# Kernel tuning notes

Hardware: AMD Instinct MI355X
Metric: run time of the kernel (lower is better)

## Reference

```python
import jax, jax.numpy as jnp
import numpy as np

B, H, L, N, F = 32, 256, 2048, 64, 32  # batch, d_model, seq len, d_state//2 complex modes, num_features


def setup_inputs() -> dict:
    key = jax.random.key(0)
    ks = jax.random.split(key, 16)
    inp = {
        "x": jax.random.normal(ks[0], (B, H, L), jnp.float32),
        "t": jax.random.normal(ks[1], (B, H), jnp.float32),
        "features": jax.random.normal(ks[2], (B, F, L), jnp.float32),
        # time_linear
        "Wt": jax.random.normal(ks[3], (H, H), jnp.float32) / np.sqrt(H),
        "bt": jnp.zeros((H,), jnp.float32),
        # LayerNorm over d_model
        "ln_g": jnp.ones((H,), jnp.float32),
        "ln_b": jnp.zeros((H,), jnp.float32),
        # S4 (diagonal / S4D parameterization, d_state=128 -> N=64 complex, bidirectional)
        "log_dt": jnp.log(jnp.full((H,), 0.01, jnp.float32))
                  + jax.random.uniform(ks[4], (H,), jnp.float32, -1.0, 1.0),
        "logA_real": jnp.log(0.5 * jnp.ones((H, N), jnp.float32)),
        "A_imag": jnp.broadcast_to(np.pi * jnp.arange(N, dtype=jnp.float32), (H, N)).copy(),
        "C_re": jax.random.normal(ks[5], (2, H, N), jnp.float32) / np.sqrt(2 * N),
        "C_im": jax.random.normal(ks[6], (2, H, N), jnp.float32) / np.sqrt(2 * N),
        "D": jax.random.normal(ks[7], (H,), jnp.float32),
        # S4 output position-wise linear
        "Wout": jax.random.normal(ks[8], (H, H), jnp.float32) / np.sqrt(H),
        "bout": jnp.zeros((H,), jnp.float32),
        # out_linear1 / out_linear2 (1x1 convs)
        "W1": jax.random.normal(ks[9], (H, H), jnp.float32) / np.sqrt(H),
        "b1": jnp.zeros((H,), jnp.float32),
        "W2": jax.random.normal(ks[10], (H, H), jnp.float32) / np.sqrt(H),
        "b2": jnp.zeros((H,), jnp.float32),
        # feature_encoder 1x1 conv
        "Wf": jax.random.normal(ks[11], (H, F), jnp.float32) / np.sqrt(F),
        "bf": jnp.zeros((H,), jnp.float32),
    }
    return inp


def _s4_block(x, t, features, Wt, bt, ln_g, ln_b, log_dt, logA_real, A_imag,
              C_re, C_im, D, Wout, bout, W1, b1, W2, b2, Wf, bf):
    Bb, Hh, Ll = x.shape
    # time conditioning: Linear(t) broadcast over length  -> (B,H,L)
    tb = t @ Wt.T + bt
    xin = x + tb[:, :, None]
    # LayerNorm over channel (d_model) axis (norm applied on transposed tensor)
    mu = jnp.mean(xin, axis=1, keepdims=True)
    var = jnp.var(xin, axis=1, keepdims=True)
    z = (xin - mu) / jnp.sqrt(var + 1e-5) * ln_g[None, :, None] + ln_b[None, :, None]
    # --- bidirectional S4 (diagonal SSM) kernel ---
    dt = jnp.exp(log_dt)                       # (H,)
    A = -jnp.exp(logA_real) + 1j * A_imag      # (H,N)
    dtA = dt[:, None] * A                      # (H,N)
    Cd = (C_re + 1j * C_im) * (jnp.exp(dtA) - 1.0) / A      # (2,H,N) discretized C
    vand = jnp.exp(dtA[:, :, None] * jnp.arange(Ll))         # (H,N,L) Vandermonde
    K = 2.0 * jnp.real(jnp.einsum('chn,hnl->chl', Cd, vand))  # (2,H,L)
    zeros = jnp.zeros_like(K[0])
    k = jnp.concatenate([K[0], zeros], -1) + jnp.concatenate([zeros, K[1][:, ::-1]], -1)  # (H,2L)
    # FFT global convolution
    y = jnp.fft.irfft(jnp.fft.rfft(z, 2 * Ll) * jnp.fft.rfft(k, 2 * Ll)[None], 2 * Ll)[..., :Ll]
    y = y + z * D[None, :, None]
    y = jax.nn.gelu(y)
    y = jnp.einsum('bhl,gh->bgl', y, Wout) + bout[None, :, None]
    xr = y + xin                                # residual inside S4Layer
    # feature encoder + gated activation
    out = xr + jnp.einsum('bfl,hf->bhl', features, Wf) + bf[None, :, None]
    g = jnp.tanh(out) * jax.nn.sigmoid(out)
    o1 = jnp.einsum('bhl,gh->bgl', g, W1) + b1[None, :, None]
    o2 = jnp.einsum('bhl,gh->bgl', g, W2) + b2[None, :, None]
    return (o1 + x, o2)


def reference(x, t, features, Wt, bt, ln_g, ln_b, log_dt, logA_real, A_imag,
              C_re, C_im, D, Wout, bout, W1, b1, W2, b2, Wf, bf):
    return _s4_block(x, t, features, Wt, bt, ln_g, ln_b, log_dt, logA_real, A_imag,
                     C_re, C_im, D, Wout, bout, W1, b1, W2, b2, Wf, bf)
```

## Files before the change

### kernel.cpp

```cpp
#include <hip/hip_runtime.h>

typedef unsigned short ushort_t;

#define Bb 32
#define Hh 256
#define Ll 2048
#define Nn 64
#define BHL 16777216

typedef __bf16 bf16x8 __attribute__((ext_vector_type(8)));
typedef float f32x4 __attribute__((ext_vector_type(4)));
typedef unsigned int uint4v __attribute__((ext_vector_type(4)));

__device__ __forceinline__ ushort_t f2bf(float f) {
    unsigned int u = __float_as_uint(f);
    unsigned int r = ((u >> 16) & 1u) + 0x7fffu;
    return (ushort_t)((u + r) >> 16);
}
__device__ __forceinline__ float bf2f(ushort_t h) {
    return __uint_as_float(((unsigned int)h) << 16);
}
__device__ __forceinline__ float gelu_tanh(float v) {
    float u = 0.7978845608028654f * fmaf(0.044715f * v, v * v, v);
    float e = __expf(2.f * u);
    float th = 1.f - 2.f / (e + 1.f);
    return 0.5f * v * (1.f + th);
}
__device__ __forceinline__ float gate_fn(float v) {
    float sg = 1.f / (1.f + __expf(-v));
    float e2 = __expf(2.f * v);
    float th = 1.f - 2.f / (e2 + 1.f);
    return th * sg;
}
__device__ __forceinline__ uint4v rev8v(uint4v a) {
    union { uint4v v; ushort_t s8[8]; } x, y;
    x.v = a;
    #pragma unroll
    for (int j = 0; j < 8; ++j) y.s8[j] = x.s8[7 - j];
    return y.v;
}

__global__ __launch_bounds__(256) void prep_kernel(
    const float* __restrict__ t, const float* __restrict__ Wt, const float* __restrict__ bt,
    const float* __restrict__ Wout, const float* __restrict__ Wf,
    const float* __restrict__ bout, const float* __restrict__ bfb,
    const float* __restrict__ W1, const float* __restrict__ b1,
    const float* __restrict__ W2, const float* __restrict__ b2,
    float* __restrict__ tb, float* __restrict__ bc, float* __restrict__ b12,
    ushort_t* __restrict__ wcf, ushort_t* __restrict__ w12f)
{
    int bx = blockIdx.x, tid = threadIdx.x;
    __shared__ float trow[256];
    if (bx < 32) {
        trow[tid] = t[bx * 256 + tid];
        __syncthreads();
        float acc = bt[tid];
        #pragma unroll 4
        for (int hh = 0; hh < 256; ++hh) acc = fmaf(trow[hh], Wt[tid * 256 + hh], acc);
        tb[bx * 256 + tid] = acc;
    } else if (bx < 64) {
        int gt = (bx - 32) * 256 + tid;
        if (gt < 256) bc[gt] = bout[gt] + bfb[gt];
        if (gt < 512) b12[gt] = (gt < 256) ? b1[gt] : b2[gt - 256];
        for (int fg = gt; fg < 9216; fg += 8192) {
            int mt = fg / 576, rem = fg % 576;
            int kc = rem >> 6, lane = rem & 63;
            int m = mt * 16 + (lane & 15);
            int kb = kc * 32 + (lane >> 4) * 8;
            #pragma unroll
            for (int j = 0; j < 8; ++j) {
                int k = kb + j;
                float v = (k < 256) ? Wout[m * 256 + k] : Wf[m * 32 + (k - 256)];
                wcf[(size_t)fg * 8 + j] = f2bf(v);
            }
        }
    } else {
        int gt = (bx - 64) * 256 + tid;
        for (int fg = gt; fg < 16384; fg += 8192) {
            int mt = fg >> 9, rem = fg & 511;
            int kc = rem >> 6, lane = rem & 63;
            int m = mt * 16 + (lane & 15);
            int kb = kc * 32 + (lane >> 4) * 8;
            #pragma unroll
            for (int j = 0; j < 8; ++j) {
                int k = kb + j;
                float v = (m < 256) ? W1[m * 256 + k] : W2[(m - 256) * 256 + k];
                w12f[(size_t)fg * 8 + j] = f2bf(v);
            }
        }
    }
}

__global__ __launch_bounds__(256) void prep2_kernel(
    const float* __restrict__ log_dt, const float* __restrict__ logA, const float* __restrict__ Aimg,
    const float* __restrict__ C_re, const float* __restrict__ C_im,
    float* __restrict__ drg, float* __restrict__ dig,
    ushort_t* __restrict__ Mfrag, ushort_t* __restrict__ Vfrag)
{
    int bx = blockIdx.x, tid = threadIdx.x;
    int h = bx >> 1, dir = bx & 1;
    __shared__ float drL[64], diL[64], crL[64], ciL[64];
    __shared__ float ktab[128];
    __shared__ ushort_t bndL[128 * 128];
    if (tid < 64) {
        int n = tid;
        int idx = h * 64 + n;
        float dt = __expf(log_dt[h]);
        float Ar = -__expf(logA[idx]);
        float Ai = Aimg[idx];
        float dr = dt * Ar, di = dt * Ai;
        float er = __expf(dr);
        float wr_ = er * __cosf(di), wi_ = er * __sinf(di);
        float nr = wr_ - 1.f, ni = wi_;
        float inv = 1.f / (Ar * Ar + Ai * Ai);
        float qr = (nr * Ar + ni * Ai) * inv;
        float qi = (ni * Ar - nr * Ai) * inv;
        float cr = C_re[dir * 16384 + idx], ci = C_im[dir * 16384 + idx];
        drL[n] = dr; diL[n] = di;
        crL[n] = 2.f * (cr * qr - ci * qi);
        ciL[n] = 2.f * (cr * qi + ci * qr);
        if (dir == 0) { drg[idx] = dr; dig[idx] = di; }
    }
    __syncthreads();
    if (tid < 128) {
        int i = tid;
        float e = (float)(i + 1 - dir);
        #pragma unroll 4
        for (int n = 0; n < 64; ++n) {
            float ex = __expf(e * drL[n]);
            float ph = e * diL[n];
            float pr = ex * __cosf(ph), pi = ex * __sinf(ph);
            bndL[i * 128 + n]      = f2bf(crL[n] * pr - ciL[n] * pi);
            bndL[i * 128 + 64 + n] = f2bf(-(crL[n] * pi + ciL[n] * pr));
        }
    } else {
        int d = tid - 128;
        float e = (float)d;
        float acc = 0.f;
        #pragma unroll 4
        for (int n = 0; n < 64; ++n) {
            float ex = __expf(e * drL[n]);
            float ph = e * diL[n];
            acc += crL[n] * (ex * __cosf(ph)) - ciL[n] * (ex * __sinf(ph));
        }
        ktab[d] = acc;
    }
    __syncthreads();
    size_t base = (size_t)bx << 15;
    for (int idx = tid; idx < 32768; idx += 256) {
        int j = idx & 7, lane = (idx >> 3) & 63, kc = (idx >> 9) & 7, mt = idx >> 12;
        int m = mt * 16 + (lane & 15);
        int k = kc * 32 + (lane >> 4) * 8 + j;
        float v;
        if (k < 128) {
            int d = m - k - dir;
            v = (d >= 0) ? ktab[d] : 0.f;
        } else {
            v = bf2f(bndL[m * 128 + (k - 128)]);
        }
        Mfrag[base + idx] = f2bf(v);
    }
    if (dir == 0) {
        size_t vbase = (size_t)h << 14;
        for (int idx = tid; idx < 16384; idx += 256) {
            int j = idx & 7, lane = (idx >> 3) & 63, kc = (idx >> 9) & 3, mt = idx >> 11;
            int s = mt * 16 + (lane & 15);
            int k = kc * 32 + (lane >> 4) * 8 + j;
            int n = s & 63;
            float e = (float)(127 - k);
            float ex = __expf(e * drL[n]);
            float ph = e * diL[n];
            float v = (s < 64) ? ex * __cosf(ph) : ex * __sinf(ph);
            Vfrag[vbase + idx] = f2bf(v);
        }
    }
}

__global__ __launch_bounds__(256) void ln_kernel(
    const float* __restrict__ x, const float* __restrict__ tb,
    const float* __restrict__ ln_g, const float* __restrict__ ln_b,
    ushort_t* __restrict__ zbf)
{
    int gid = blockIdx.x * 256 + threadIdx.x;
    int b = gid >> 11, l = gid & 2047;
    const float* xp = x + (size_t)b * (Hh * Ll) + l;
    const float* tbp = tb + b * 256;
    float sum = 0.f, ssq = 0.f;
    #pragma unroll 8
    for (int h = 0; h < 256; ++h) {
        float v = xp[(size_t)h * Ll] + tbp[h];
        sum += v; ssq = fmaf(v, v, ssq);
    }
    float mean = sum * (1.f / 256.f);
    float var = fmaf(ssq, 1.f / 256.f, -mean * mean);
    float rstd = rsqrtf(var + 1e-5f);
    ushort_t* zp = zbf + (size_t)b * (Hh * Ll) + l;
    #pragma unroll 8
    for (int h = 0; h < 256; ++h) {
        float v = xp[(size_t)h * Ll] + tbp[h];
        zp[(size_t)h * Ll] = f2bf((v - mean) * rstd * ln_g[h] + ln_b[h]);
    }
}

__global__ __launch_bounds__(256) void ssm_mega_kernel(
    const ushort_t* __restrict__ zbf,
    const float* __restrict__ drg, const float* __restrict__ dig, const float* __restrict__ Dv,
    const ushort_t* __restrict__ Mfrag, const ushort_t* __restrict__ Vfrag,
    ushort_t* __restrict__ ya)
{
    __shared__ ushort_t Zs[64 * 136];
    __shared__ ushort_t Ssf[64 * 136];
    __shared__ ushort_t Ssb[64 * 136];
    __shared__ float Qb[2 * 128 * 17];
    int tid = threadIdx.x, lane = tid & 63, w = tid >> 6;
    int q = lane >> 4, cl = lane & 15;
    int h = blockIdx.x, cb = blockIdx.y;
    int b0 = cb * 4;
    for (int i = tid; i < 1024; i += 256) {
        int bsub = i >> 8, t8 = (i & 255) * 8;
        const ushort_t* zrow = zbf + ((size_t)((b0 + bsub) * 256 + h) << 11);
        *(uint4v*)&Zs[(bsub * 16 + (t8 >> 7)) * 136 + (t8 & 127)] = *(const uint4v*)(zrow + t8);
    }
    float dr0 = drg[h * 64 + lane], di0 = dig[h * 64 + lane];
    float ex128 = __expf(128.f * dr0);
    float w128r = ex128 * __cosf(128.f * di0);
    float w128i = ex128 * __sinf(128.f * di0);
    float Dh = Dv[h];
    __syncthreads();
    const ushort_t* vbase = Vfrag + ((size_t)h << 14);
    const ushort_t* mbase0 = Mfrag + ((size_t)(h * 2) << 15);
    const ushort_t* mbase1 = Mfrag + ((size_t)(h * 2 + 1) << 15);
    for (int bsub = 0; bsub < 4; ++bsub) {
        f32x4 qa[2][2] = {};
        #pragma unroll
        for (int kc = 0; kc < 4; ++kc) {
            int kk = kc * 32 + q * 8;
            bf16x8 bz = __builtin_bit_cast(bf16x8,
                *(const uint4v*)&Zs[(bsub * 16 + cl) * 136 + kk]);
            bf16x8 bzr = __builtin_bit_cast(bf16x8, rev8v(
                *(const uint4v*)&Zs[(bsub * 16 + (15 - cl)) * 136 + (120 - kk)]));
            #pragma unroll
            for (int i = 0; i < 2; ++i) {
                int mt = w * 2 + i;
                bf16x8 af = __builtin_bit_cast(bf16x8,
                    *(const uint4v*)(vbase + (((mt * 4 + kc) * 64 + lane) << 3)));
                qa[0][i] = __builtin_amdgcn_mfma_f32_16x16x32_bf16(af, bz, qa[0][i], 0, 0, 0);
                qa[1][i] = __builtin_amdgcn_mfma_f32_16x16x32_bf16(af, bzr, qa[1][i], 0, 0, 0);
            }
        }
        __syncthreads();
        #pragma unroll
        for (int d = 0; d < 2; ++d)
            #pragma unroll
            for (int i = 0; i < 2; ++i) {
                int mt = w * 2 + i;
                #pragma unroll
                for (int r = 0; r < 4; ++r)
                    Qb[d * 2176 + (mt * 16 + q * 4 + r) * 17 + cl] = qa[d][i][r];
            }
        __syncthreads();
        if (w < 2) {
            ushort_t* S = (w == 0) ? Ssf : Ssb;
            const float* Qp = Qb + w * 2176;
            float sre = 0.f, sim = 0.f;
            for (int cc = 0; cc < 16; ++cc) {
                S[(bsub * 16 + cc) * 136 + lane] = f2bf(sre);
                S[(bsub * 16 + cc) * 136 + 64 + lane] = f2bf(sim);
                float qre = Qp[lane * 17 + cc];
                float qim = Qp[(64 + lane) * 17 + cc];
                float nre = fmaf(w128r, sre, fmaf(-w128i, sim, qre));
                float nim = fmaf(w128r, sim, fmaf(w128i, sre, qim));
                sre = nre; sim = nim;
            }
        }
        __syncthreads();
    }
    f32x4 accf[2][4] = {}, accb[2][4] = {};
    for (int kc = 0; kc < 8; ++kc) {
        int kk = (kc & 3) * 32 + q * 8;
        bf16x8 aff[2], afb[2];
        #pragma unroll
        for (int i = 0; i < 2; ++i) {
            int mt = w * 2 + i;
            aff[i] = __builtin_bit_cast(bf16x8, *(const uint4v*)(mbase0 + (((mt * 8 + kc) * 64 + lane) << 3)));
            afb[i] = __builtin_bit_cast(bf16x8, *(const uint4v*)(mbase1 + (((mt * 8 + kc) * 64 + lane) << 3)));
        }
        #pragma unroll
        for (int nt = 0; nt < 4; ++nt) {
            bf16x8 bff, bfb_;
            if (kc < 4) {
                bff  = __builtin_bit_cast(bf16x8, *(const uint4v*)&Zs[(nt * 16 + cl) * 136 + kk]);
                bfb_ = __builtin_bit_cast(bf16x8, rev8v(
                       *(const uint4v*)&Zs[(nt * 16 + (15 - cl)) * 136 + (120 - kk)]));
            } else {
                bff  = __builtin_bit_cast(bf16x8, *(const uint4v*)&Ssf[(nt * 16 + cl) * 136 + kk]);
                bfb_ = __builtin_bit_cast(bf16x8, *(const uint4v*)&Ssb[(nt * 16 + cl) * 136 + kk]);
            }
            #pragma unroll
            for (int i = 0; i < 2; ++i) {
                accf[i][nt] = __builtin_amdgcn_mfma_f32_16x16x32_bf16(aff[i], bff,  accf[i][nt], 0, 0, 0);
                accb[i][nt] = __builtin_amdgcn_mfma_f32_16x16x32_bf16(afb[i], bfb_, accb[i][nt], 0, 0, 0);
            }
        }
    }
    __syncthreads();
    ushort_t* Yf = Ssf;
    ushort_t* Yb = Ssb;
    #pragma unroll
    for (int i = 0; i < 2; ++i) {
        int mt = w * 2 + i;
        #pragma unroll
        for (int nt = 0; nt < 4; ++nt) {
            int col = nt * 16 + cl;
            #pragma unroll
            for (int r = 0; r < 4; ++r) {
                int m = mt * 16 + q * 4 + r;
                Yf[col * 136 + m] = f2bf(accf[i][nt][r]);
                Yb[col * 136 + m] = f2bf(accb[i][nt][r]);
            }
        }
    }
    __syncthreads();
    for (int u = tid; u < 1024; u += 256) {
        int col = u >> 4, i0 = (u & 15) * 8;
        int bsub = col >> 4, c = col & 15;
        int colb = bsub * 16 + (15 - c);
        union { uint4v v; ushort_t s8[8]; } uf, uz, ub, uo;
        uf.v = *(const uint4v*)&Yf[col * 136 + i0];
        uz.v = *(const uint4v*)&Zs[col * 136 + i0];
        ub.v = rev8v(*(const uint4v*)&Yb[colb * 136 + (120 - i0)]);
        #pragma unroll
        for (int j = 0; j < 8; ++j) {
            float v = bf2f(uf.s8[j]) + bf2f(ub.s8[j]) + Dh * bf2f(uz.s8[j]);
            uo.s8[j] = f2bf(gelu_tanh(v));
        }
        ushort_t* yrow = ya + ((size_t)((b0 + bsub) * 256 + h) << 11);
        *(uint4v*)(yrow + c * 128 + i0) = uo.v;
    }
}

__global__ __launch_bounds__(256, 4) void gemm1_kernel(
    const ushort_t* __restrict__ ya, const float* __restrict__ feat,
    const float* __restrict__ x, const float* __restrict__ tb,
    const float* __restrict__ bc, const ushort_t* __restrict__ wcf,
    ushort_t* __restrict__ g)
{
    __shared__ __align__(16) ushort_t XT[64 * 48];
    int tid = threadIdx.x;
    int w = tid >> 6, lane = tid & 63;
    int bx = blockIdx.x;
    int b = bx >> 5;
    int l0 = (bx & 31) << 6;
    f32x4 acc[4][4] = {};
    int kk = tid >> 3, ng = tid & 7;
    for (int kc = 0; kc < 9; ++kc) {
        int k = kc * 32 + kk;
        union { uint4v v; ushort_t s[8]; } u;
        if (k < 256) {
            u.v = *(const uint4v*)(ya + ((size_t)(b * 256 + k) << 11) + l0 + ng * 8);
        } else {
            const float* src = feat + (size_t)(b * 32 + (k - 256)) * Ll + l0 + ng * 8;
            #pragma unroll
            for (int j = 0; j < 8; ++j) u.s[j] = f2bf(src[j]);
        }
        #pragma unroll
        for (int j = 0; j < 8; ++j) XT[(ng * 8 + j) * 48 + kk] = u.s[j];
        __syncthreads();
        bf16x8 af[4], bfr[4];
        #pragma unroll
        for (int i = 0; i < 4; ++i) {
            const ushort_t* p = wcf + ((size_t)((w * 4 + i) * 9 + kc) * 64 + lane) * 8;
            af[i] = __builtin_bit_cast(bf16x8, *(const uint4v*)p);
        }
        #pragma unroll
        for (int nt = 0; nt < 4; ++nt) {
            const ushort_t* p = &XT[(nt * 16 + (lane & 15)) * 48 + (lane >> 4) * 8];
            bfr[nt] = __builtin_bit_cast(bf16x8, *(const uint4v*)p);
        }
        #pragma unroll
        for (int i = 0; i < 4; ++i)
            #pragma unroll
            for (int nt = 0; nt < 4; ++nt)
                acc[i][nt] = __builtin_amdgcn_mfma_f32_16x16x32_bf16(af[i], bfr[nt], acc[i][nt], 0, 0, 0);
        __syncthreads();
    }
    int q = lane >> 4, nl = lane & 15;
    #pragma unroll
    for (int i = 0; i < 4; ++i) {
        #pragma unroll
        for (int nt = 0; nt < 4; ++nt) {
            int n = l0 + nt * 16 + nl;
            #pragma unroll
            for (int r = 0; r < 4; ++r) {
                int m = (w * 4 + i) * 16 + q * 4 + r;
                size_t oi = (size_t)(b * 256 + m) * Ll + n;
                float v = acc[i][nt][r] + bc[m] + tb[b * 256 + m] + x[oi];
                g[oi] = f2bf(gate_fn(v));
            }
        }
    }
}

__global__ __launch_bounds__(256, 4) void gemm2_kernel(
    const ushort_t* __restrict__ g, const float* __restrict__ x,
    const float* __restrict__ b12, const ushort_t* __restrict__ w12f,
    float* __restrict__ out)
{
    __shared__ __align__(16) ushort_t XT[64 * 48];
    int tid = threadIdx.x;
    int w = tid >> 6, lane = tid & 63;
    int bx = blockIdx.x;
    int half = blockIdx.y;
    int b = bx >> 5;
    int l0 = (bx & 31) << 6;
    f32x4 acc[4][4] = {};
    int kk = tid >> 3, ng = tid & 7;
    for (int kc = 0; kc < 8; ++kc) {
        int k = kc * 32 + kk;
        union { uint4v v; ushort_t s[8]; } u;
        u.v = *(const uint4v*)(g + (size_t)(b * 256 + k) * Ll + l0 + ng * 8);
        #pragma unroll
        for (int j = 0; j < 8; ++j) XT[(ng * 8 + j) * 48 + kk] = u.s[j];
        __syncthreads();
        bf16x8 af[4], bfr[4];
        #pragma unroll
        for (int i = 0; i < 4; ++i) {
            int mtg = half * 16 + w * 4 + i;
            const ushort_t* p = w12f + ((size_t)(mtg * 8 + kc) * 64 + lane) * 8;
            af[i] = __builtin_bit_cast(bf16x8, *(const uint4v*)p);
        }
        #pragma unroll
        for (int nt = 0; nt < 4; ++nt) {
            const ushort_t* p = &XT[(nt * 16 + (lane & 15)) * 48 + (lane >> 4) * 8];
            bfr[nt] = __builtin_bit_cast(bf16x8, *(const uint4v*)p);
        }
        #pragma unroll
        for (int i = 0; i < 4; ++i)
            #pragma unroll
            for (int nt = 0; nt < 4; ++nt)
                acc[i][nt] = __builtin_amdgcn_mfma_f32_16x16x32_bf16(af[i], bfr[nt], acc[i][nt], 0, 0, 0);
        __syncthreads();
    }
    int q = lane >> 4, nl = lane & 15;
    #pragma unroll
    for (int i = 0; i < 4; ++i) {
        #pragma unroll
        for (int nt = 0; nt < 4; ++nt) {
            int n = l0 + nt * 16 + nl;
            #pragma unroll
            for (int r = 0; r < 4; ++r) {
                int m = (w * 4 + i) * 16 + q * 4 + r;
                size_t oi = (size_t)(b * 256 + m) * Ll + n;
                float v = acc[i][nt][r] + b12[half * 256 + m];
                if (half == 0) out[oi] = v + x[oi];
                else out[(size_t)BHL + oi] = v;
            }
        }
    }
}

extern "C" void kernel_launch(void* const* d_in, const int* in_sizes, int n_in,
                              void* d_out, int out_size, void* d_ws, size_t ws_size,
                              hipStream_t stream) {
    const float* x      = (const float*)d_in[0];
    const float* t      = (const float*)d_in[1];
    const float* feat   = (const float*)d_in[2];
    const float* Wt     = (const float*)d_in[3];
    const float* bt     = (const float*)d_in[4];
    const float* ln_g   = (const float*)d_in[5];
    const float* ln_b   = (const float*)d_in[6];
    const float* log_dt = (const float*)d_in[7];
    const float* logA   = (const float*)d_in[8];
    const float* Aimg   = (const float*)d_in[9];
    const float* C_re   = (const float*)d_in[10];
    const float* C_im   = (const float*)d_in[11];
    const float* Dv     = (const float*)d_in[12];
    const float* Wout   = (const float*)d_in[13];
    const float* bout   = (const float*)d_in[14];
    const float* W1     = (const float*)d_in[15];
    const float* b1     = (const float*)d_in[16];
    const float* W2     = (const float*)d_in[17];
    const float* b2     = (const float*)d_in[18];
    const float* Wf     = (const float*)d_in[19];
    const float* bfb    = (const float*)d_in[20];

    char* ob = (char*)d_out;
    ushort_t* zbf = (ushort_t*)ob;
    ushort_t* yab = (ushort_t*)(ob + 33554432);
    float*    out = (float*)d_out;

    char* ws = (char*)d_ws;
    ushort_t* Mfrag = (ushort_t*)ws;
    ushort_t* gbuf  = (ushort_t*)ws;
    ushort_t* Vfrag = (ushort_t*)(ws + 33554432);
    char* ws2 = ws + 33554432 + 8388608;
    float* tb   = (float*)ws2;
    float* drg  = (float*)(ws2 + 32768);
    float* dig  = (float*)(ws2 + 98304);
    float* bc   = (float*)(ws2 + 163840);
    float* b12  = (float*)(ws2 + 164864);
    ushort_t* wcf  = (ushort_t*)(ws2 + 166912);
    ushort_t* w12f = (ushort_t*)(ws2 + 314368);

    prep_kernel<<<96, 256, 0, stream>>>(t, Wt, bt, Wout, Wf, bout, bfb, W1, b1, W2, b2,
                                        tb, bc, b12, wcf, w12f);
    prep2_kernel<<<512, 256, 0, stream>>>(log_dt, logA, Aimg, C_re, C_im, drg, dig, Mfrag, Vfrag);
    ln_kernel<<<256, 256, 0, stream>>>(x, tb, ln_g, ln_b, zbf);
    ssm_mega_kernel<<<dim3(256, 8), 256, 0, stream>>>(zbf, drg, dig, Dv, Mfrag, Vfrag, yab);
    gemm1_kernel<<<1024, 256, 0, stream>>>(yab, feat, x, tb, bc, wcf, gbuf);
    gemm2_kernel<<<dim3(1024, 2), 256, 0, stream>>>(gbuf, x, b12, w12f, out);
}
```

Before: 426.2 us.

## Fuse gated-activation GEMM with output GEMMs and tile LayerNorm through LDS

Adds gemm12_kernel, which computes the feature/S4 projection and gate, keeps the gated tile in shared memory, and then runs the W1/W2 output GEMMs in the same block. This removes the round-trip of the bf16 g buffer through global memory and one kernel launch, at the cost of higher LDS use and register pressure (launch bounds 2). The fused path is only used when the workspace is large enough, since yab moves into the workspace. LayerNorm is also restructured: each block stages a 256x64 tile in LDS with float4 loads and does a 4-way partial reduction, so x is read once and coalesced instead of twice with strided per-thread loads.

Measured after the change: 535.4 us. 1.26x slower.

```diff
diff --git a/kernel.cpp b/kernel.cpp
--- a/kernel.cpp
+++ b/kernel.cpp
@@ -181,23 +181,43 @@
     const float* __restrict__ ln_g, const float* __restrict__ ln_b,
     ushort_t* __restrict__ zbf)
 {
-    int gid = blockIdx.x * 256 + threadIdx.x;
-    int b = gid >> 11, l = gid & 2047;
-    const float* xp = x + (size_t)b * (Hh * Ll) + l;
+    __shared__ float Xs[256][65];
+    __shared__ float rs[4][64], rq[4][64];
+    int tid = threadIdx.x, bx = blockIdx.x;
+    int b = bx >> 5, l0 = (bx & 31) << 6;
+    const float* xb = x + (size_t)b * (Hh * (size_t)Ll) + l0;
     const float* tbp = tb + b * 256;
+    int f4 = tid & 15, h0 = tid >> 4;
+    #pragma unroll
+    for (int i = 0; i < 16; ++i) {
+        int h = i * 16 + h0;
+        float4 v = *((const float4*)(xb + (size_t)h * Ll) + f4);
+        float tv = tbp[h];
+        Xs[h][f4 * 4 + 0] = v.x + tv;
+        Xs[h][f4 * 4 + 1] = v.y + tv;
+        Xs[h][f4 * 4 + 2] = v.z + tv;
+        Xs[h][f4 * 4 + 3] = v.w + tv;
+    }
+    __syncthreads();
+    int l = tid & 63, qd = tid >> 6;
     float sum = 0.f, ssq = 0.f;
     #pragma unroll 8
-    for (int h = 0; h < 256; ++h) {
-        float v = xp[(size_t)h * Ll] + tbp[h];
+    for (int i = 0; i < 64; ++i) {
+        float v = Xs[qd * 64 + i][l];
         sum += v; ssq = fmaf(v, v, ssq);
     }
+    rs[qd][l] = sum; rq[qd][l] = ssq;
+    __syncthreads();
+    sum = rs[0][l] + rs[1][l] + rs[2][l] + rs[3][l];
+    ssq = rq[0][l] + rq[1][l] + rq[2][l] + rq[3][l];
     float mean = sum * (1.f / 256.f);
     float var = fmaf(ssq, 1.f / 256.f, -mean * mean);
     float rstd = rsqrtf(var + 1e-5f);
-    ushort_t* zp = zbf + (size_t)b * (Hh * Ll) + l;
+    ushort_t* zp = zbf + (size_t)b * (Hh * (size_t)Ll) + l0 + l;
     #pragma unroll 8
-    for (int h = 0; h < 256; ++h) {
-        float v = xp[(size_t)h * Ll] + tbp[h];
+    for (int i = 0; i < 64; ++i) {
+        int h = qd * 64 + i;
+        float v = Xs[h][l];
         zp[(size_t)h * Ll] = f2bf((v - mean) * rstd * ln_g[h] + ln_b[h]);
     }
 }
@@ -336,6 +356,113 @@
         }
         ushort_t* yrow = ya + ((size_t)((b0 + bsub) * 256 + h) << 11);
         *(uint4v*)(yrow + c * 128 + i0) = uo.v;
+    }
+}
+
+__global__ __launch_bounds__(256, 2) void gemm12_kernel(
+    const ushort_t* __restrict__ ya, const float* __restrict__ feat,
+    const float* __restrict__ x, const float* __restrict__ tb,
+    const float* __restrict__ bc, const ushort_t* __restrict__ wcf,
+    const float* __restrict__ b12, const ushort_t* __restrict__ w12f,
+    float* __restrict__ out)
+{
+    __shared__ __align__(16) ushort_t XT[64 * 48];
+    __shared__ __align__(16) ushort_t Gs[64][264];
+    int tid = threadIdx.x;
+    int w = tid >> 6, lane = tid & 63;
+    int bx = blockIdx.x;
+    int b = bx >> 5;
+    int l0 = (bx & 31) << 6;
+    f32x4 acc[4][4] = {};
+    int kk = tid >> 3, ng = tid & 7;
+    for (int kc = 0; kc < 9; ++kc) {
+        int k = kc * 32 + kk;
+        union { uint4v v; ushort_t s[8]; } u;
+        if (k < 256) {
+            u.v = *(const uint4v*)(ya + ((size_t)(b * 256 + k) << 11) + l0 + ng * 8);
+        } else {
+            const float* src = feat + (size_t)(b * 32 + (k - 256)) * Ll + l0 + ng * 8;
+            #pragma unroll
+            for (int j = 0; j < 8; ++j) u.s[j] = f2bf(src[j]);
+        }
+        #pragma unroll
+        for (int j = 0; j < 8; ++j) XT[(ng * 8 + j) * 48 + kk] = u.s[j];
+        __syncthreads();
+        bf16x8 af[4], bfr[4];
+        #pragma unroll
+        for (int i = 0; i < 4; ++i) {
+            const ushort_t* p = wcf + ((size_t)((w * 4 + i) * 9 + kc) * 64 + lane) * 8;
+            af[i] = __builtin_bit_cast(bf16x8, *(const uint4v*)p);
+        }
+        #pragma unroll
+        for (int nt = 0; nt < 4; ++nt) {
+            const ushort_t* p = &XT[(nt * 16 + (lane & 15)) * 48 + (lane >> 4) * 8];
+            bfr[nt] = __builtin_bit_cast(bf16x8, *(const uint4v*)p);
+        }
+        #pragma unroll
+        for (int i = 0; i < 4; ++i)
+            #pragma unroll
+            for (int nt = 0; nt < 4; ++nt)
+                acc[i][nt] = __builtin_amdgcn_mfma_f32_16x16x32_bf16(af[i], bfr[nt], acc[i][nt], 0, 0, 0);
+        __syncthreads();
+    }
+    int q = lane >> 4, nl = lane & 15;
+    float xv[4][4][4];
+    #pragma unroll
+    for (int i = 0; i < 4; ++i) {
+        #pragma unroll
+        for (int nt = 0; nt < 4; ++nt) {
+            int n = l0 + nt * 16 + nl;
+            union { unsigned long long u; ushort_t s[4]; } gw;
+            #pragma unroll
+            for (int r = 0; r < 4; ++r) {
+                int m = (w * 4 + i) * 16 + q * 4 + r;
+                size_t oi = (size_t)(b * 256 + m) * Ll + n;
+                float xvv = x[oi];
+                xv[i][nt][r] = xvv;
+                float v = acc[i][nt][r] + bc[m] + tb[b * 256 + m] + xvv;
+                gw.s[r] = f2bf(gate_fn(v));
+            }
+            *(unsigned long long*)&Gs[nt * 16 + nl][(w * 4 + i) * 16 + q * 4] = gw.u;
+        }
+    }
+    __syncthreads();
+    #pragma unroll 1
+    for (int half = 0; half < 2; ++half) {
+        f32x4 a2[4][4] = {};
+        for (int kc = 0; kc < 8; ++kc) {
+            bf16x8 af[4], bfr[4];
+            #pragma unroll
+            for (int i = 0; i < 4; ++i) {
+                int mtg = half * 16 + w * 4 + i;
+                const ushort_t* p = w12f + ((size_t)(mtg * 8 + kc) * 64 + lane) * 8;
+                af[i] = __builtin_bit_cast(bf16x8, *(const uint4v*)p);
+            }
+            #pragma unroll
+            for (int nt = 0; nt < 4; ++nt)
+                bfr[nt] = __builtin_bit_cast(bf16x8,
+                    *(const uint4v*)&Gs[nt * 16 + (lane & 15)][kc * 32 + (lane >> 4) * 8]);
+            #pragma unroll
+            for (int i = 0; i < 4; ++i)
+                #pragma unroll
+                for (int nt = 0; nt < 4; ++nt)
+                    a2[i][nt] = __builtin_amdgcn_mfma_f32_16x16x32_bf16(af[i], bfr[nt], a2[i][nt], 0, 0, 0);
+        }
+        #pragma unroll
+        for (int i = 0; i < 4; ++i) {
+            #pragma unroll
+            for (int nt = 0; nt < 4; ++nt) {
+                int n = l0 + nt * 16 + nl;
+                #pragma unroll
+                for (int r = 0; r < 4; ++r) {
+                    int m = (w * 4 + i) * 16 + q * 4 + r;
+                    size_t oi = (size_t)(b * 256 + m) * Ll + n;
+                    float v = a2[i][nt][r] + b12[half * 256 + m];
+                    if (half == 0) out[oi] = v + xv[i][nt][r];
+                    else out[(size_t)BHL + oi] = v;
+                }
+            }
+        }
     }
 }
 
@@ -486,14 +613,22 @@
 
     char* ob = (char*)d_out;
     ushort_t* zbf = (ushort_t*)ob;
-    ushort_t* yab = (ushort_t*)(ob + 33554432);
     float*    out = (float*)d_out;
 
     char* ws = (char*)d_ws;
     ushort_t* Mfrag = (ushort_t*)ws;
-    ushort_t* gbuf  = (ushort_t*)ws;
     ushort_t* Vfrag = (ushort_t*)(ws + 33554432);
-    char* ws2 = ws + 33554432 + 8388608;
+    size_t fused_need = 33554432ull + 8388608ull + 33554432ull + 1048576ull;
+    bool fused = (ws_size >= fused_need);
+    ushort_t* yab;
+    char* ws2;
+    if (fused) {
+        yab = (ushort_t*)(ws + 33554432 + 8388608);
+        ws2 = ws + 33554432 + 8388608 + 33554432;
+    } else {
+        yab = (ushort_t*)(ob + 33554432);
+        ws2 = ws + 33554432 + 8388608;
+    }
     float* tb   = (float*)ws2;
     float* drg  = (float*)(ws2 + 32768);
     float* dig  = (float*)(ws2 + 98304);
@@ -505,8 +640,13 @@
     prep_kernel<<<96, 256, 0, stream>>>(t, Wt, bt, Wout, Wf, bout, bfb, W1, b1, W2, b2,
                                         tb, bc, b12, wcf, w12f);
     prep2_kernel<<<512, 256, 0, stream>>>(log_dt, logA, Aimg, C_re, C_im, drg, dig, Mfrag, Vfrag);
-    ln_kernel<<<256, 256, 0, stream>>>(x, tb, ln_g, ln_b, zbf);
+    ln_kernel<<<1024, 256, 0, stream>>>(x, tb, ln_g, ln_b, zbf);
     ssm_mega_kernel<<<dim3(256, 8), 256, 0, stream>>>(zbf, drg, dig, Dv, Mfrag, Vfrag, yab);
-    gemm1_kernel<<<1024, 256, 0, stream>>>(yab, feat, x, tb, bc, wcf, gbuf);
-    gemm2_kernel<<<dim3(1024, 2), 256, 0, stream>>>(gbuf, x, b12, w12f, out);
-}
+    if (fused) {
+        gemm12_kernel<<<1024, 256, 0, stream>>>(yab, feat, x, tb, bc, wcf, b12, w12f, out);
+    } else {
+        ushort_t* gbuf = (ushort_t*)ws;
+        gemm1_kernel<<<1024, 256, 0, stream>>>(yab, feat, x, tb, bc, wcf, gbuf);
+        gemm2_kernel<<<dim3(1024, 2), 256, 0, stream>>>(gbuf, x, b12, w12f, out);
+    }
+}
```
